# Kernel optimization log

Measured on AMD Instinct MI355X. Metric: run time of the kernel, lower is better.

The kernel has to match this reference:

```python
import jax, jax.numpy as jnp
import numpy as np

B, S, D = 64, 1024, 256
N_HEADS = 1
HEAD_DIM = D // N_HEADS
MASK_VAL = -10000.0


def setup_inputs() -> dict:
    key = jax.random.key(0)
    k1, k2, k3 = jax.random.split(key, 3)
    x = jax.random.normal(k1, (B, S, D), dtype=jnp.float32)
    W_qkv = jax.random.normal(k2, (D, 3 * D), dtype=jnp.float32) * 0.02
    b_qkv = jnp.zeros((3 * D,), dtype=jnp.float32)
    W_out = jax.random.normal(k3, (D, D), dtype=jnp.float32) * 0.02
    b_out = jnp.zeros((D,), dtype=jnp.float32)
    return {"x": x, "W_qkv": W_qkv, "b_qkv": b_qkv, "W_out": W_out, "b_out": b_out}


def reference(x, W_qkv, b_qkv, W_out, b_out):
    # QKV projection: [B,S,3D]
    qkv = jnp.einsum('bsd,df->bsf', x, W_qkv) + b_qkv
    q, k, v = jnp.split(qkv, 3, axis=2)
    # split heads -> [B,H,S,hd] (H=1)
    def split_heads(t):
        return t.reshape(B, S, N_HEADS, HEAD_DIM).transpose(0, 2, 1, 3)
    q, k, v = split_heads(q), split_heads(k), split_heads(v)
    # scaled scores [B,H,S,S]
    scores = jnp.einsum('bhqd,bhkd->bhqk', q, k) / jnp.sqrt(jnp.float32(HEAD_DIM))
    causal = jnp.tril(jnp.ones((1, 1, S, S), dtype=bool))
    scores = jnp.where(causal, scores, jnp.float32(MASK_VAL))
    attn = jax.nn.softmax(scores, axis=-1)  # dropout deterministic (training=False)
    out = jnp.einsum('bhqk,bhkd->bhqd', attn, v)
    # merge heads -> [B,S,D]
    out = out.transpose(0, 2, 1, 3).reshape(B, S, D)
    out = jnp.einsum('bsd,de->bse', out, W_out) + b_out
    return out, attn
```

## Files before the change

### kernel.cpp

```cpp
#include <hip/hip_runtime.h>
#include <hip/hip_bf16.h>

#define BB 64
#define SS 1024
#define DDIM 256

typedef unsigned short u16;
typedef __attribute__((ext_vector_type(4))) float f4;
typedef __attribute__((ext_vector_type(8))) short bf16x8;
typedef __attribute__((ext_vector_type(4))) short bf16x4;
typedef __attribute__((ext_vector_type(4))) float f32x4;

__device__ inline u16 f2b(float f) {
  unsigned int u = __float_as_uint(f);
  unsigned int r = (u + 0x7fffu + ((u >> 16) & 1u)) >> 16;
  return (u16)r;
}

#define GLOAD16(g, l)                                                  \
  __builtin_amdgcn_global_load_lds(                                    \
      (const __attribute__((address_space(1))) void*)(g),              \
      (__attribute__((address_space(3))) void*)(l), 16, 0, 0)

__global__ __launch_bounds__(256) void cast_x(const float* __restrict__ x,
                                              u16* __restrict__ xb, int n8) {
  int i = blockIdx.x * 256 + threadIdx.x;
  const int stride = gridDim.x * 256;
  for (; i < n8; i += stride) {
    f4 a = ((const f4*)x)[2 * i];
    f4 b = ((const f4*)x)[2 * i + 1];
    bf16x8 o;
    o[0] = f2b(a[0]); o[1] = f2b(a[1]); o[2] = f2b(a[2]); o[3] = f2b(a[3]);
    o[4] = f2b(b[0]); o[5] = f2b(b[1]); o[6] = f2b(b[2]); o[7] = f2b(b[3]);
    ((bf16x8*)xb)[i] = o;
  }
}

__global__ __launch_bounds__(256) void cast_w(const float* __restrict__ Wqkv,
                                              const float* __restrict__ Wout,
                                              u16* __restrict__ Wqkvt,
                                              u16* __restrict__ Woutt) {
  int t = blockIdx.x * 256 + threadIdx.x;
  if (t < 256 * 768) {
    int k = t / 768, n = t % 768;
    Wqkvt[n * 256 + k] = f2b(Wqkv[t]);
  }
  if (t < 256 * 256) {
    int k = t / 256, n = t % 256;
    Woutt[n * 256 + k] = f2b(Wout[t]);
  }
}

template <int EPI, int NXT>
__global__ __launch_bounds__(256) void gemm_mfma(
    const u16* __restrict__ A, const u16* __restrict__ Bt,
    const float* __restrict__ bias, float* __restrict__ outF,
    u16* __restrict__ Qb, u16* __restrict__ Kb, u16* __restrict__ Vt) {
  __shared__ u16 As[128 * 64];
  __shared__ u16 Bs[128 * 64];
  const int t = threadIdx.x;
  const int w = t >> 6, l = t & 63;
  const int lr = l & 15, lg = l >> 4;
  const int id = blockIdx.x;
  const int r8 = id & 7;
  const int tt = id >> 3;
  const int xt = tt % NXT;
  const int yt = (tt / NXT) * 8 + r8;
  const int m0 = yt * 128, n0 = xt * 128;
  const int wm = (w >> 1) * 64, wn = (w & 1) * 64;

  f32x4 acc[4][4] = {};

  for (int k0 = 0; k0 < 256; k0 += 64) {
    __syncthreads();
#pragma unroll
    for (int j = 0; j < 4; ++j) {
      int idx = t + j * 256;
      int row = idx >> 3, c = idx & 7;
      f4 va = *(const f4*)&A[(size_t)(m0 + row) * 256 + k0 + c * 8];
      *(f4*)&As[row * 64 + ((c ^ (row & 7)) * 8)] = va;
      f4 vb = *(const f4*)&Bt[(size_t)(n0 + row) * 256 + k0 + c * 8];
      *(f4*)&Bs[row * 64 + ((c ^ (row & 7)) * 8)] = vb;
    }
    __syncthreads();
#pragma unroll
    for (int kc = 0; kc < 2; ++kc) {
      bf16x8 af[4], bfr[4];
#pragma unroll
      for (int f = 0; f < 4; ++f) {
        int ar = wm + f * 16 + lr;
        af[f] = *(const bf16x8*)&As[ar * 64 + (((kc * 4 + lg) ^ (ar & 7)) * 8)];
        int br = wn + f * 16 + lr;
        bfr[f] = *(const bf16x8*)&Bs[br * 64 + (((kc * 4 + lg) ^ (br & 7)) * 8)];
      }
#pragma unroll
      for (int i = 0; i < 4; ++i)
#pragma unroll
        for (int jn = 0; jn < 4; ++jn)
          acc[i][jn] = __builtin_amdgcn_mfma_f32_16x16x32_bf16(
              af[i], bfr[jn], acc[i][jn], 0, 0, 0);
    }
  }

#pragma unroll
  for (int i = 0; i < 4; ++i) {
    const int mbase = m0 + wm + i * 16 + lg * 4;
#pragma unroll
    for (int jn = 0; jn < 4; ++jn) {
      const int n = n0 + wn + jn * 16 + lr;
      const float bv = bias[n];
      if (EPI == 0) {
#pragma unroll
        for (int r = 0; r < 4; ++r)
          outF[(size_t)(mbase + r) * 256 + n] = acc[i][jn][r] + bv;
      } else {
        if (n < 256) {
#pragma unroll
          for (int r = 0; r < 4; ++r)
            Qb[(size_t)(mbase + r) * 256 + n] = f2b(acc[i][jn][r] + bv);
        } else if (n < 512) {
#pragma unroll
          for (int r = 0; r < 4; ++r)
            Kb[(size_t)(mbase + r) * 256 + (n - 256)] = f2b(acc[i][jn][r] + bv);
        } else {
          const int d = n - 512;
          const int b = mbase >> 10, sl = mbase & 1023;
          bf16x4 pk;
#pragma unroll
          for (int r = 0; r < 4; ++r) pk[r] = f2b(acc[i][jn][r] + bv);
          *(bf16x4*)&Vt[((size_t)b * 256 + d) * 1024 + sl] = pk;
        }
      }
    }
  }
}

__global__ __launch_bounds__(256) void attn_fused(
    const u16* __restrict__ Qg, const u16* __restrict__ Kg,
    const u16* __restrict__ Vtg, float* __restrict__ attn,
    u16* __restrict__ outa) {
  __shared__ u16 pool[35328];
  u16* Ks = pool;
  u16* Vs = pool + 16384;
  u16* Ps = pool + 32768;

  const int t = threadIdx.x;
  const int w = t >> 6, l = t & 63;
  const int lr = l & 15, lg = l >> 4;
  const int id = blockIdx.x;
  const int b = (id & 7) * 8 + ((id >> 3) & 7);
  const int pair = id >> 6;
  const int qta = pair, qtb = 15 - pair;
  const int d0w = w * 64;

  const u16* Kbase = Kg + (size_t)b * SS * DDIM;
  const u16* Vbase = Vtg + (size_t)b * DDIM * SS;

  auto stageK64 = [&](int kt, int buf) {
#pragma unroll
    for (int i = 0; i < 8; ++i) {
      const int rr = 16 * w + 2 * i + (l >> 5);
      const int chunk = l & 31;
      const int csrc = (chunk & 24) | ((chunk & 7) ^ (rr & 7));
      const u16* g = Kbase + (size_t)(kt * 64 + rr) * DDIM + csrc * 8;
      GLOAD16(g, pool + buf * 16384 + (16 * w + 2 * i) * 256);
    }
  };
  auto stageK = [&](int kt, int buf) {
    const int rbase = 8 * w;
#pragma unroll
    for (int i = 0; i < 4; ++i) {
      const int rr = rbase + 2 * i + (l >> 5);
      const int chunk = l & 31;
      const int csrc = (chunk & 24) | ((chunk & 7) ^ (rr & 7));
      const u16* g = Kbase + (size_t)(kt * 32 + rr) * DDIM + csrc * 8;
      GLOAD16(g, Ks + buf * 8192 + (rbase + 2 * i) * 256);
    }
  };
  auto stageV = [&](int kt, int buf) {
    const int dbase = 64 * w;
#pragma unroll
    for (int i = 0; i < 4; ++i) {
      const int dd = dbase + 16 * i + (l >> 2);
      const u16* g = Vbase + (size_t)dd * SS + kt * 32 + (l & 3) * 8;
      GLOAD16(g, Vs + buf * 8192 + (dbase + 16 * i) * 32);
    }
  };
  auto loadQ = [&](int qt, bf16x8* qf) {
    const u16* qb = Qg + ((size_t)(b * SS + qt * 64 + w * 16 + lr)) * DDIM;
#pragma unroll
    for (int kc = 0; kc < 8; ++kc)
      qf[kc] = *(const bf16x8*)&qb[kc * 32 + lg * 8];
  };

  bf16x8 qfA[8], qfB[8];
  loadQ(qta, qfA);
  loadQ(qtb, qfB);
  float raA[4] = {0.f, 0.f, 0.f, 0.f}, raB[4] = {0.f, 0.f, 0.f, 0.f};

  stageK64(0, 0);
  __syncthreads();
  for (int kt = 0; kt <= qtb; ++kt) {
    const int buf = kt & 1;
    if (kt < qtb) stageK64(kt + 1, buf ^ 1);
    const bool doA = (kt <= qta);
#pragma unroll
    for (int sf = 0; sf < 4; ++sf) {
      const int srow = sf * 16 + lr;
      const u16* kr = pool + buf * 16384 + srow * 256;
      f32x4 sA = {0.f, 0.f, 0.f, 0.f}, sB = {0.f, 0.f, 0.f, 0.f};
#pragma unroll
      for (int kc = 0; kc < 8; ++kc) {
        const int c = kc * 4 + lg;
        const int ch = (c & 24) | ((c & 7) ^ (srow & 7));
        bf16x8 bfr = *(const bf16x8*)&kr[ch * 8];
        sB = __builtin_amdgcn_mfma_f32_16x16x32_bf16(qfB[kc], bfr, sB, 0, 0, 0);
        if (doA)
          sA = __builtin_amdgcn_mfma_f32_16x16x32_bf16(qfA[kc], bfr, sA, 0, 0, 0);
      }
      const int scol = kt * 64 + sf * 16 + lr;
      {
        const int qrow = qtb * 64 + w * 16 + lg * 4;
#pragma unroll
        for (int r = 0; r < 4; ++r)
          raB[r] += (scol <= qrow + r) ? __expf(sB[r] * 0.0625f) : 0.f;
      }
      if (doA) {
        const int qrow = qta * 64 + w * 16 + lg * 4;
#pragma unroll
        for (int r = 0; r < 4; ++r)
          raA[r] += (scol <= qrow + r) ? __expf(sA[r] * 0.0625f) : 0.f;
      }
    }
    __syncthreads();
  }
#pragma unroll
  for (int m = 1; m < 16; m <<= 1) {
#pragma unroll
    for (int r = 0; r < 4; ++r) {
      raA[r] += __shfl_xor(raA[r], m, 64);
      raB[r] += __shfl_xor(raB[r], m, 64);
    }
  }
  float invA[4], invB[4];
#pragma unroll
  for (int r = 0; r < 4; ++r) {
    invA[r] = 1.0f / raA[r];
    invB[r] = 1.0f / raB[r];
  }

  for (int tile = 0; tile < 2; ++tile) {
    const int qt = tile ? qtb : qta;
    const int last = 2 * qt + 1;
    bf16x8 qf[8];
    loadQ(qt, qf);
    float inv[4];
#pragma unroll
    for (int r = 0; r < 4; ++r) inv[r] = tile ? invB[r] : invA[r];
    f32x4 oacc[4][4];
#pragma unroll
    for (int qb = 0; qb < 4; ++qb)
#pragma unroll
      for (int df = 0; df < 4; ++df) oacc[qb][df] = (f32x4){0.f, 0.f, 0.f, 0.f};

    float* attnw = attn + ((size_t)(b * SS + qt * 64 + w * 16)) * SS;

    __syncthreads();
    stageK(0, 0);
    stageV(0, 0);
    __syncthreads();

    for (int kt = 0; kt <= last; ++kt) {
      const int buf = kt & 1;
#pragma unroll
      for (int sf = 0; sf < 2; ++sf) {
        const int srow = sf * 16 + lr;
        const u16* kr = Ks + buf * 8192 + srow * 256;
        f32x4 s = {0.f, 0.f, 0.f, 0.f};
#pragma unroll
        for (int kc = 0; kc < 8; ++kc) {
          const int c = kc * 4 + lg;
          const int ch = (c & 24) | ((c & 7) ^ (srow & 7));
          bf16x8 bfr = *(const bf16x8*)&kr[ch * 8];
          s = __builtin_amdgcn_mfma_f32_16x16x32_bf16(qf[kc], bfr, s, 0, 0, 0);
        }
        const int scol = kt * 32 + sf * 16 + lr;
        const int qrow = qt * 64 + w * 16 + lg * 4;
#pragma unroll
        for (int r = 0; r < 4; ++r) {
          const float e = (scol <= qrow + r) ? __expf(s[r] * 0.0625f) : 0.f;
          Ps[(w * 16 + lg * 4 + r) * 40 + sf * 16 + lr] = f2b(e * inv[r]);
        }
      }
#pragma unroll
      for (int g2 = 0; g2 < 2; ++g2) {
        const int row = g2 * 8 + (l >> 3);
        const int col = (l & 7) * 4;
        bf16x4 pv = *(const bf16x4*)&Ps[(w * 16 + row) * 40 + col];
        f4 o;
#pragma unroll
        for (int j = 0; j < 4; ++j)
          o[j] = __uint_as_float(((unsigned)(u16)pv[j]) << 16);
        *(f4*)&attnw[(size_t)row * SS + kt * 32 + col] = o;
      }
      __syncthreads();
      if (kt < last) {
        stageK(kt + 1, buf ^ 1);
        stageV(kt + 1, buf ^ 1);
      }
      bf16x8 vfr[4];
      const u16* vb = Vs + buf * 8192;
#pragma unroll
      for (int df = 0; df < 4; ++df)
        vfr[df] = *(const bf16x8*)&vb[(d0w + df * 16 + lr) * 32 + lg * 8];
#pragma unroll
      for (int qb = 0; qb < 4; ++qb) {
        bf16x8 pa = *(const bf16x8*)&Ps[(qb * 16 + lr) * 40 + lg * 8];
#pragma unroll
        for (int df = 0; df < 4; ++df)
          oacc[qb][df] = __builtin_amdgcn_mfma_f32_16x16x32_bf16(
              pa, vfr[df], oacc[qb][df], 0, 0, 0);
      }
      __syncthreads();
    }

    {
      const f4 z = {0.f, 0.f, 0.f, 0.f};
      for (int c0 = (qt + 1) * 64; c0 < SS; c0 += 32) {
#pragma unroll
        for (int g2 = 0; g2 < 2; ++g2) {
          const int row = g2 * 8 + (l >> 3);
          *(f4*)&attnw[(size_t)row * SS + c0 + (l & 7) * 4] = z;
        }
      }
    }

#pragma unroll
    for (int qb = 0; qb < 4; ++qb)
#pragma unroll
      for (int df = 0; df < 4; ++df)
#pragma unroll
        for (int r = 0; r < 4; ++r)
          pool[(qb * 16 + lg * 4 + r) * 264 + d0w + df * 16 + lr] =
              f2b(oacc[qb][df][r]);
    __syncthreads();
    {
      const size_t obase = (size_t)(b * SS + qt * 64);
#pragma unroll
      for (int i = 0; i < 8; ++i) {
        const int row = w * 16 + 2 * i + (l >> 5);
        bf16x8 v = *(const bf16x8*)&pool[row * 264 + (l & 31) * 8];
        *(bf16x8*)&outa[(obase + row) * DDIM + (l & 31) * 8] = v;
      }
    }
  }
}

extern "C" void kernel_launch(void* const* d_in, const int* in_sizes, int n_in,
                              void* d_out, int out_size, void* d_ws,
                              size_t ws_size, hipStream_t stream) {
  const float* x    = (const float*)d_in[0];
  const float* Wqkv = (const float*)d_in[1];
  const float* bqkv = (const float*)d_in[2];
  const float* Wout = (const float*)d_in[3];
  const float* bout = (const float*)d_in[4];

  float* out  = (float*)d_out;
  float* attn = out + (size_t)BB * SS * DDIM;

  const size_t NTOK = (size_t)BB * SS;
  u16* ws = (u16*)d_ws;
  u16* xb    = ws;
  u16* Qb    = xb + NTOK * DDIM;
  u16* Kb    = Qb + NTOK * DDIM;
  u16* Vt    = Kb + NTOK * DDIM;
  u16* outa  = Vt + NTOK * DDIM;
  u16* Wqkvt = outa + NTOK * DDIM;
  u16* Woutt = Wqkvt + 768 * 256;

  cast_x<<<2048, 256, 0, stream>>>(x, xb, (int)(NTOK * DDIM / 8));
  cast_w<<<768, 256, 0, stream>>>(Wqkv, Wout, Wqkvt, Woutt);

  gemm_mfma<1, 6><<<3072, 256, 0, stream>>>(xb, Wqkvt, bqkv, nullptr, Qb, Kb,
                                            Vt);
  attn_fused<<<512, 256, 0, stream>>>(Qb, Kb, Vt, attn, outa);
  gemm_mfma<0, 2><<<1024, 256, 0, stream>>>(outa, Woutt, bout, out, nullptr,
                                            nullptr, nullptr);
}
```

Before: 255.1 us.

## Process both query tiles concurrently with 512-thread blocks sharing K/V stages

Doubles the attention block to 8 waves, with one 4-wave group handling the early query tile and the other the late tile. The two groups now run concurrently over shared K and V staging instead of two sequential tile passes, so each K/V tile is loaded once per block rather than reloaded per query tile. Staging is moved ahead of compute so the next tile prefetches during the current one, and block order is remapped to interleave short and long pairs. The short-tile group idles once its causal range ends, and the larger block needs more registers and LDS, which may limit occupancy.

```diff
diff --git a/kernel.cpp b/kernel.cpp
--- a/kernel.cpp
+++ b/kernel.cpp
@@ -135,143 +135,124 @@
   }
 }
 
-__global__ __launch_bounds__(256) void attn_fused(
+__global__ __launch_bounds__(512) void attn_fused(
     const u16* __restrict__ Qg, const u16* __restrict__ Kg,
     const u16* __restrict__ Vtg, float* __restrict__ attn,
     u16* __restrict__ outa) {
-  __shared__ u16 pool[35328];
+  __shared__ u16 pool[37888];
   u16* Ks = pool;
   u16* Vs = pool + 16384;
   u16* Ps = pool + 32768;
 
   const int t = threadIdx.x;
   const int w = t >> 6, l = t & 63;
+  const int g = w >> 2, wg = w & 3;
   const int lr = l & 15, lg = l >> 4;
   const int id = blockIdx.x;
-  const int b = (id & 7) * 8 + ((id >> 3) & 7);
-  const int pair = id >> 6;
+  const int b = 8 * (id & 7) + ((id >> 3) & 7);
+  const int z = id >> 6;
+  const int pair = (z < 4) ? z : (11 - z);
   const int qta = pair, qtb = 15 - pair;
-  const int d0w = w * 64;
+  const int qt = g ? qtb : qta;
+  const int lastA = 2 * qta + 1, lastB = 2 * qtb + 1;
+  const int d0 = wg * 64;
 
   const u16* Kbase = Kg + (size_t)b * SS * DDIM;
   const u16* Vbase = Vtg + (size_t)b * DDIM * SS;
 
   auto stageK64 = [&](int kt, int buf) {
 #pragma unroll
-    for (int i = 0; i < 8; ++i) {
-      const int rr = 16 * w + 2 * i + (l >> 5);
+    for (int i = 0; i < 4; ++i) {
+      const int rr = 8 * w + 2 * i + (l >> 5);
       const int chunk = l & 31;
       const int csrc = (chunk & 24) | ((chunk & 7) ^ (rr & 7));
-      const u16* g = Kbase + (size_t)(kt * 64 + rr) * DDIM + csrc * 8;
-      GLOAD16(g, pool + buf * 16384 + (16 * w + 2 * i) * 256);
+      const u16* gp = Kbase + (size_t)(kt * 64 + rr) * DDIM + csrc * 8;
+      GLOAD16(gp, pool + buf * 16384 + (8 * w + 2 * i) * 256);
     }
   };
   auto stageK = [&](int kt, int buf) {
-    const int rbase = 8 * w;
-#pragma unroll
-    for (int i = 0; i < 4; ++i) {
-      const int rr = rbase + 2 * i + (l >> 5);
+#pragma unroll
+    for (int i = 0; i < 2; ++i) {
+      const int rr = 4 * w + 2 * i + (l >> 5);
       const int chunk = l & 31;
       const int csrc = (chunk & 24) | ((chunk & 7) ^ (rr & 7));
-      const u16* g = Kbase + (size_t)(kt * 32 + rr) * DDIM + csrc * 8;
-      GLOAD16(g, Ks + buf * 8192 + (rbase + 2 * i) * 256);
+      const u16* gp = Kbase + (size_t)(kt * 32 + rr) * DDIM + csrc * 8;
+      GLOAD16(gp, Ks + buf * 8192 + (4 * w + 2 * i) * 256);
     }
   };
   auto stageV = [&](int kt, int buf) {
-    const int dbase = 64 * w;
-#pragma unroll
-    for (int i = 0; i < 4; ++i) {
-      const int dd = dbase + 16 * i + (l >> 2);
-      const u16* g = Vbase + (size_t)dd * SS + kt * 32 + (l & 3) * 8;
-      GLOAD16(g, Vs + buf * 8192 + (dbase + 16 * i) * 32);
+#pragma unroll
+    for (int i = 0; i < 2; ++i) {
+      const int dd = 32 * w + 16 * i + (l >> 2);
+      const u16* gp = Vbase + (size_t)dd * SS + kt * 32 + (l & 3) * 8;
+      GLOAD16(gp, Vs + buf * 8192 + (32 * w + 16 * i) * 32);
     }
   };
-  auto loadQ = [&](int qt, bf16x8* qf) {
-    const u16* qb = Qg + ((size_t)(b * SS + qt * 64 + w * 16 + lr)) * DDIM;
+
+  bf16x8 qf[8];
+  {
+    const u16* qb = Qg + ((size_t)(b * SS + qt * 64 + wg * 16 + lr)) * DDIM;
 #pragma unroll
     for (int kc = 0; kc < 8; ++kc)
       qf[kc] = *(const bf16x8*)&qb[kc * 32 + lg * 8];
-  };
-
-  bf16x8 qfA[8], qfB[8];
-  loadQ(qta, qfA);
-  loadQ(qtb, qfB);
-  float raA[4] = {0.f, 0.f, 0.f, 0.f}, raB[4] = {0.f, 0.f, 0.f, 0.f};
-
+  }
+
+  float ra[4] = {0.f, 0.f, 0.f, 0.f};
   stageK64(0, 0);
   __syncthreads();
   for (int kt = 0; kt <= qtb; ++kt) {
     const int buf = kt & 1;
     if (kt < qtb) stageK64(kt + 1, buf ^ 1);
-    const bool doA = (kt <= qta);
-#pragma unroll
-    for (int sf = 0; sf < 4; ++sf) {
-      const int srow = sf * 16 + lr;
-      const u16* kr = pool + buf * 16384 + srow * 256;
-      f32x4 sA = {0.f, 0.f, 0.f, 0.f}, sB = {0.f, 0.f, 0.f, 0.f};
-#pragma unroll
-      for (int kc = 0; kc < 8; ++kc) {
-        const int c = kc * 4 + lg;
-        const int ch = (c & 24) | ((c & 7) ^ (srow & 7));
-        bf16x8 bfr = *(const bf16x8*)&kr[ch * 8];
-        sB = __builtin_amdgcn_mfma_f32_16x16x32_bf16(qfB[kc], bfr, sB, 0, 0, 0);
-        if (doA)
-          sA = __builtin_amdgcn_mfma_f32_16x16x32_bf16(qfA[kc], bfr, sA, 0, 0, 0);
-      }
-      const int scol = kt * 64 + sf * 16 + lr;
-      {
-        const int qrow = qtb * 64 + w * 16 + lg * 4;
+    if (g == 1 || kt <= qta) {
+#pragma unroll
+      for (int sf = 0; sf < 4; ++sf) {
+        const int srow = sf * 16 + lr;
+        const u16* kr = pool + buf * 16384 + srow * 256;
+        f32x4 s = {0.f, 0.f, 0.f, 0.f};
+#pragma unroll
+        for (int kc = 0; kc < 8; ++kc) {
+          const int c = kc * 4 + lg;
+          const int ch = (c & 24) | ((c & 7) ^ (srow & 7));
+          bf16x8 bfr = *(const bf16x8*)&kr[ch * 8];
+          s = __builtin_amdgcn_mfma_f32_16x16x32_bf16(qf[kc], bfr, s, 0, 0, 0);
+        }
+        const int scol = kt * 64 + sf * 16 + lr;
+        const int qrow = qt * 64 + wg * 16 + lg * 4;
 #pragma unroll
         for (int r = 0; r < 4; ++r)
-          raB[r] += (scol <= qrow + r) ? __expf(sB[r] * 0.0625f) : 0.f;
-      }
-      if (doA) {
-        const int qrow = qta * 64 + w * 16 + lg * 4;
-#pragma unroll
-        for (int r = 0; r < 4; ++r)
-          raA[r] += (scol <= qrow + r) ? __expf(sA[r] * 0.0625f) : 0.f;
-      }
-    }
-    __syncthreads();
-  }
-#pragma unroll
-  for (int m = 1; m < 16; m <<= 1) {
-#pragma unroll
-    for (int r = 0; r < 4; ++r) {
-      raA[r] += __shfl_xor(raA[r], m, 64);
-      raB[r] += __shfl_xor(raB[r], m, 64);
-    }
-  }
-  float invA[4], invB[4];
-#pragma unroll
-  for (int r = 0; r < 4; ++r) {
-    invA[r] = 1.0f / raA[r];
-    invB[r] = 1.0f / raB[r];
-  }
-
-  for (int tile = 0; tile < 2; ++tile) {
-    const int qt = tile ? qtb : qta;
-    const int last = 2 * qt + 1;
-    bf16x8 qf[8];
-    loadQ(qt, qf);
-    float inv[4];
-#pragma unroll
-    for (int r = 0; r < 4; ++r) inv[r] = tile ? invB[r] : invA[r];
-    f32x4 oacc[4][4];
-#pragma unroll
-    for (int qb = 0; qb < 4; ++qb)
-#pragma unroll
-      for (int df = 0; df < 4; ++df) oacc[qb][df] = (f32x4){0.f, 0.f, 0.f, 0.f};
-
-    float* attnw = attn + ((size_t)(b * SS + qt * 64 + w * 16)) * SS;
-
-    __syncthreads();
-    stageK(0, 0);
-    stageV(0, 0);
-    __syncthreads();
-
-    for (int kt = 0; kt <= last; ++kt) {
-      const int buf = kt & 1;
+          ra[r] += (scol <= qrow + r) ? __expf(s[r] * 0.0625f) : 0.f;
+      }
+    }
+    __syncthreads();
+  }
+#pragma unroll
+  for (int m = 1; m < 16; m <<= 1)
+#pragma unroll
+    for (int r = 0; r < 4; ++r) ra[r] += __shfl_xor(ra[r], m, 64);
+  float inv[4];
+#pragma unroll
+  for (int r = 0; r < 4; ++r) inv[r] = 1.0f / ra[r];
+
+  f32x4 oacc[4][4];
+#pragma unroll
+  for (int qb = 0; qb < 4; ++qb)
+#pragma unroll
+    for (int df = 0; df < 4; ++df) oacc[qb][df] = (f32x4){0.f, 0.f, 0.f, 0.f};
+
+  float* attnw = attn + ((size_t)(b * SS + qt * 64 + wg * 16)) * SS;
+
+  stageK(0, 0);
+  stageV(0, 0);
+  __syncthreads();
+
+  for (int kt = 0; kt <= lastB; ++kt) {
+    const int buf = kt & 1;
+    if (kt < lastB) {
+      stageK(kt + 1, buf ^ 1);
+      stageV(kt + 1, buf ^ 1);
+    }
+    const bool act = (g == 1) || (kt <= lastA);
+    if (act) {
 #pragma unroll
       for (int sf = 0; sf < 2; ++sf) {
         const int srow = sf * 16 + lr;
@@ -285,7 +266,7 @@
           s = __builtin_amdgcn_mfma_f32_16x16x32_bf16(qf[kc], bfr, s, 0, 0, 0);
         }
         const int scol = kt * 32 + sf * 16 + lr;
-        const int qrow = qt * 64 + w * 16 + lg * 4;
+        const int qrow = qt * 64 + wg * 16 + lg * 4;
 #pragma unroll
         for (int r = 0; r < 4; ++r) {
           const float e = (scol <= qrow + r) ? __expf(s[r] * 0.0625f) : 0.f;
@@ -303,55 +284,54 @@
           o[j] = __uint_as_float(((unsigned)(u16)pv[j]) << 16);
         *(f4*)&attnw[(size_t)row * SS + kt * 32 + col] = o;
       }
-      __syncthreads();
-      if (kt < last) {
-        stageK(kt + 1, buf ^ 1);
-        stageV(kt + 1, buf ^ 1);
-      }
+    }
+    __syncthreads();
+    if (act) {
       bf16x8 vfr[4];
       const u16* vb = Vs + buf * 8192;
 #pragma unroll
       for (int df = 0; df < 4; ++df)
-        vfr[df] = *(const bf16x8*)&vb[(d0w + df * 16 + lr) * 32 + lg * 8];
+        vfr[df] = *(const bf16x8*)&vb[(d0 + df * 16 + lr) * 32 + lg * 8];
 #pragma unroll
       for (int qb = 0; qb < 4; ++qb) {
-        bf16x8 pa = *(const bf16x8*)&Ps[(qb * 16 + lr) * 40 + lg * 8];
+        bf16x8 pa = *(const bf16x8*)&Ps[((g * 4 + qb) * 16 + lr) * 40 + lg * 8];
 #pragma unroll
         for (int df = 0; df < 4; ++df)
           oacc[qb][df] = __builtin_amdgcn_mfma_f32_16x16x32_bf16(
               pa, vfr[df], oacc[qb][df], 0, 0, 0);
       }
-      __syncthreads();
-    }
-
-    {
-      const f4 z = {0.f, 0.f, 0.f, 0.f};
-      for (int c0 = (qt + 1) * 64; c0 < SS; c0 += 32) {
-#pragma unroll
-        for (int g2 = 0; g2 < 2; ++g2) {
-          const int row = g2 * 8 + (l >> 3);
-          *(f4*)&attnw[(size_t)row * SS + c0 + (l & 7) * 4] = z;
-        }
-      }
-    }
-
-#pragma unroll
-    for (int qb = 0; qb < 4; ++qb)
-#pragma unroll
-      for (int df = 0; df < 4; ++df)
-#pragma unroll
-        for (int r = 0; r < 4; ++r)
-          pool[(qb * 16 + lg * 4 + r) * 264 + d0w + df * 16 + lr] =
-              f2b(oacc[qb][df][r]);
-    __syncthreads();
-    {
-      const size_t obase = (size_t)(b * SS + qt * 64);
-#pragma unroll
-      for (int i = 0; i < 8; ++i) {
-        const int row = w * 16 + 2 * i + (l >> 5);
-        bf16x8 v = *(const bf16x8*)&pool[row * 264 + (l & 31) * 8];
-        *(bf16x8*)&outa[(obase + row) * DDIM + (l & 31) * 8] = v;
-      }
+    }
+    __syncthreads();
+  }
+
+  {
+    const f4 zf = {0.f, 0.f, 0.f, 0.f};
+    for (int c0 = (qt + 1) * 64; c0 < SS; c0 += 32) {
+#pragma unroll
+      for (int g2 = 0; g2 < 2; ++g2) {
+        const int row = g2 * 8 + (l >> 3);
+        *(f4*)&attnw[(size_t)row * SS + c0 + (l & 7) * 4] = zf;
+      }
+    }
+  }
+
+#pragma unroll
+  for (int qb = 0; qb < 4; ++qb)
+#pragma unroll
+    for (int df = 0; df < 4; ++df)
+#pragma unroll
+      for (int r = 0; r < 4; ++r)
+        pool[(g * 64 + qb * 16 + lg * 4 + r) * 264 + d0 + df * 16 + lr] =
+            f2b(oacc[qb][df][r]);
+  __syncthreads();
+  {
+#pragma unroll
+    for (int i = 0; i < 8; ++i) {
+      const int row = w * 16 + 2 * i + (l >> 5);
+      const int qtt = (row >> 6) ? qtb : qta;
+      const size_t grow = (size_t)(b * SS + qtt * 64 + (row & 63));
+      bf16x8 v = *(const bf16x8*)&pool[row * 264 + (l & 31) * 8];
+      *(bf16x8*)&outa[grow * DDIM + (l & 31) * 8] = v;
     }
   }
 }
@@ -383,7 +363,7 @@
 
   gemm_mfma<1, 6><<<3072, 256, 0, stream>>>(xb, Wqkvt, bqkv, nullptr, Qb, Kb,
                                             Vt);
-  attn_fused<<<512, 256, 0, stream>>>(Qb, Kb, Vt, attn, outa);
+  attn_fused<<<512, 512, 0, stream>>>(Qb, Kb, Vt, attn, outa);
   gemm_mfma<0, 2><<<1024, 256, 0, stream>>>(outa, Woutt, bout, out, nullptr,
                                             nullptr, nullptr);
 }
```

Result: no change. 257.7 us (+1.0%).
